# Performance work log

Hardware: AMD Instinct MI355X
Metric: run time of the kernel (lower is better)

## Reference

```python
import jax, jax.numpy as jnp
import numpy as np

B, SEQ, DIM, HEADS = 2, 2048, 512, 8
HD = DIM // HEADS
RANK, DFF = 128, 1024
TAU_MEM, TAU_ADAPT, SLOPE, EPS = 0.99, 0.95, 25.0, 1e-6
THRESH, ADAPT_STRENGTH = 0.5, 0.1
TREE_LEVELS = int(np.log2(SEQ))  # 11


def rmsnorm(x, w, eps=EPS):
    return x * jax.lax.rsqrt(jnp.mean(x * x, axis=-1, keepdims=True) + eps) * w


def rope_cos_sin(seq, hd):
    inv = 1.0 / (10000.0 ** (jnp.arange(0, hd, 2, dtype=jnp.float32) / hd))
    f = jnp.arange(seq, dtype=jnp.float32)[:, None] * inv[None, :]  # [S, hd/2]
    emb = jnp.concatenate([f, f], axis=-1)  # [S, hd]
    return jnp.cos(emb), jnp.sin(emb)


def apply_rope(x, cos, sin):
    # x: [B, H, S, hd]; rotate-half formulation
    x1, x2 = jnp.split(x, 2, axis=-1)
    return x * cos + jnp.concatenate([-x2, x1], axis=-1) * sin


def setup_inputs() -> dict:
    key = jax.random.key(0)
    ks = jax.random.split(key, 12)
    w = lambda k, shape, fan: (jax.random.normal(k, shape, jnp.float32) / np.sqrt(fan))
    return {
        "x": jax.random.normal(ks[0], (B, SEQ, DIM), jnp.float32),
        "norm_w": jnp.ones((DIM,), jnp.float32),
        "wq": w(ks[1], (DIM, DIM), DIM),
        "wk": w(ks[2], (DIM, DIM), DIM),
        "wv": w(ks[3], (DIM, DIM), DIM),
        "wo": w(ks[4], (DIM, DIM), DIM),
        "lat_w": w(ks[5], (SEQ, SEQ), SEQ),
        "bt": jnp.full((DIM,), THRESH, jnp.float32),
        "as_w": jnp.full((DIM,), ADAPT_STRENGTH, jnp.float32),
        "gate_w": w(ks[6], (DIM, DIM), DIM),
        "tnorm1_w": jnp.ones((DIM,), jnp.float32),
        "tnorm2_w": jnp.ones((DIM,), jnp.float32),
        "ffn_norm_w": jnp.ones((DIM,), jnp.float32),
        "u_w": w(ks[7], (DIM, RANK), DIM),
        "v_w": w(ks[8], (RANK, 2 * DFF), RANK),
        "down_w": w(ks[9], (DFF, DIM), DFF),
    }


def reference(x, norm_w, wq, wk, wv, wo, lat_w, bt, as_w, gate_w,
              tnorm1_w, tnorm2_w, ffn_norm_w, u_w, v_w, down_w):
    Bx, S, D = x.shape
    # --- pre-norm + QKV projections (base_proj) ---
    h = rmsnorm(x, norm_w)
    q = (h @ wq.T).reshape(Bx, S, HEADS, HD).transpose(0, 2, 1, 3)  # [B,H,S,hd]
    k = (h @ wk.T).reshape(Bx, S, HEADS, HD).transpose(0, 2, 1, 3)
    v = (h @ wv.T).reshape(Bx, S, HEADS, HD).transpose(0, 2, 1, 3)
    # --- RoPE ---
    cos, sin = rope_cos_sin(S, HD)
    q = apply_rope(q, cos, sin)
    k = apply_rope(k, cos, sin)
    # --- causal self-attention ---
    scores = jnp.einsum("bhqd,bhkd->bhqk", q, k) / np.sqrt(HD)
    causal = jnp.tril(jnp.ones((S, S), bool))
    scores = jnp.where(causal, scores, jnp.float32(-1e9))
    attn = jnp.einsum("bhqk,bhkd->bhqd", jax.nn.softmax(scores, axis=-1), v)
    attn = attn.transpose(0, 2, 1, 3).reshape(Bx, S, D) @ wo.T
    # --- causal lateral mixing across sequence ---
    mixed = jnp.einsum("ts,bsd->btd", jnp.tril(lat_w), attn)
    # --- ALIF spiking recurrence over the sequence (soft surrogate spike) ---
    def alif_step(carry, i_t):
        vmem, ad = carry
        vmem = TAU_MEM * vmem + i_t
        th = bt + as_w * ad
        spike = jax.nn.sigmoid(SLOPE * (vmem - th))
        vmem = vmem - spike * th          # soft reset
        ad = TAU_ADAPT * ad + spike        # threshold adaptation
        return (vmem, ad), spike
    init = (jnp.zeros((Bx, D), x.dtype), jnp.zeros((Bx, D), x.dtype))
    _, spikes = jax.lax.scan(alif_step, init, mixed.transpose(1, 0, 2))
    spikes = spikes.transpose(1, 0, 2)  # [B,S,D]
    # --- fused addadd residual ---
    h2 = x + mixed + spikes
    # --- binary-tree cell recursion to a root summary ---
    s = h2
    for _ in range(TREE_LEVELS):
        raw = s[:, 0::2, :] + s[:, 1::2, :]         # pairwise sums (raw_sums)
        res = 0.5 * raw                              # residual / prev_s surrogate
        n = rmsnorm(raw, tnorm1_w)
        g = jax.nn.sigmoid(n @ gate_w.T)
        s = rmsnorm(g * n + (1.0 - g) * res, tnorm2_w)
    h3 = h2 + s[:, 0:1, :]  # broadcast root back over the sequence
    # --- low-rank SwiGLU FFN ---
    hn = rmsnorm(h3, ffn_norm_w)
    up = (hn @ u_w) @ v_w                 # [B,S,2*DFF]
    a, b = jnp.split(up, 2, axis=-1)
    ffn = (jax.nn.silu(a) * b) @ down_w   # [B,S,D]
    return h3 + ffn
```

## Files before the change

### kernel.cpp

```cpp
#include <hip/hip_runtime.h>
#include <math.h>

#define BB 2
#define SS 2048
#define DD 512
#define HH 8
#define HDD 64
#define RANKK 128
#define DFFF 1024

typedef short bf16x8 __attribute__((ext_vector_type(8)));
typedef float f32x4 __attribute__((ext_vector_type(4)));

__device__ __forceinline__ short f2b(float f) {
  union { float f; unsigned u; } v; v.f = f;
  unsigned r = v.u + 0x7FFF + ((v.u >> 16) & 1);
  return (short)(r >> 16);
}
__device__ __forceinline__ float b2f(short s) {
  union { unsigned u; float f; } v; v.u = ((unsigned)(unsigned short)s) << 16;
  return v.f;
}

__device__ __forceinline__ void gll16(const void* g, void* l) {
  __builtin_amdgcn_global_load_lds(
      (const __attribute__((address_space(1))) unsigned int*)g,
      (__attribute__((address_space(3))) unsigned int*)l, 16, 0, 0);
}

__device__ __forceinline__ float wsum(float v) {
#pragma unroll
  for (int off = 32; off > 0; off >>= 1) v += __shfl_xor(v, off, 64);
  return v;
}

__global__ void splitw(const float* __restrict__ in, short* __restrict__ hi,
                       short* __restrict__ lo, int n) {
  int i = (blockIdx.x * 256 + threadIdx.x) * 4;
  if (i >= n) return;
  float4 v = *(const float4*)(in + i);
  short4 h4, l4;
  h4.x = f2b(v.x); l4.x = f2b(v.x - b2f(h4.x));
  h4.y = f2b(v.y); l4.y = f2b(v.y - b2f(h4.y));
  h4.z = f2b(v.z); l4.z = f2b(v.z - b2f(h4.z));
  h4.w = f2b(v.w); l4.w = f2b(v.w - b2f(h4.w));
  *(short4*)(hi + i) = h4;
  *(short4*)(lo + i) = l4;
}

__global__ void cvtb(const float* __restrict__ in, short* __restrict__ out, int n) {
  int i = (blockIdx.x * 256 + threadIdx.x) * 4;
  if (i >= n) return;
  float4 v = *(const float4*)(in + i);
  short4 o; o.x = f2b(v.x); o.y = f2b(v.y); o.z = f2b(v.z); o.w = f2b(v.w);
  *(short4*)(out + i) = o;
}

__global__ void sum2(const float* __restrict__ a, const float* __restrict__ bq,
                     float* __restrict__ o) {
  int i = (blockIdx.x * 256 + threadIdx.x) * 4;
  float4 va = *(const float4*)(a + i);
  float4 vb = *(const float4*)(bq + i);
  float4 vo = {va.x + vb.x, va.y + vb.y, va.z + vb.z, va.w + vb.w};
  *(float4*)(o + i) = vo;
}

__global__ void transp_cvt(const float* __restrict__ in, short* __restrict__ out,
                           int R, int C) {
  __shared__ float t[32][33];
  int c0 = blockIdx.x * 32, r0 = blockIdx.y * 32;
#pragma unroll
  for (int i = 0; i < 4; i++) {
    int idx = threadIdx.x + i * 256;
    int r = idx >> 5, c = idx & 31;
    t[r][c] = in[(size_t)(r0 + r) * C + c0 + c];
  }
  __syncthreads();
#pragma unroll
  for (int i = 0; i < 4; i++) {
    int idx = threadIdx.x + i * 256;
    int cc = idx >> 5, rr = idx & 31;
    out[(size_t)(c0 + cc) * R + r0 + rr] = f2b(t[rr][cc]);
  }
}

__global__ void rmsnorm_hl(const float* __restrict__ x, const float* __restrict__ w,
                           short* __restrict__ oh, short* __restrict__ ol, int rows) {
  int wid = blockIdx.x * 4 + (threadIdx.x >> 6);
  int lane = threadIdx.x & 63;
  if (wid >= rows) return;
  const float* xp = x + (size_t)wid * DD + lane * 8;
  float4 a = *(const float4*)xp;
  float4 b = *(const float4*)(xp + 4);
  float ss = a.x*a.x + a.y*a.y + a.z*a.z + a.w*a.w
           + b.x*b.x + b.y*b.y + b.z*b.z + b.w*b.w;
  ss = wsum(ss);
  float r = rsqrtf(ss * (1.0f / DD) + 1e-6f);
  const float* wp = w + lane * 8;
  float4 wa = *(const float4*)wp, wb = *(const float4*)(wp + 4);
  float o8[8] = {a.x*r*wa.x, a.y*r*wa.y, a.z*r*wa.z, a.w*r*wa.w,
                 b.x*r*wb.x, b.y*r*wb.y, b.z*r*wb.z, b.w*r*wb.w};
  short hv[8], lv[8];
#pragma unroll
  for (int i = 0; i < 8; i++) { hv[i] = f2b(o8[i]); lv[i] = f2b(o8[i] - b2f(hv[i])); }
  short* op = oh + (size_t)wid * DD + lane * 8;
  short* lp = ol + (size_t)wid * DD + lane * 8;
  *(short4*)op = make_short4(hv[0], hv[1], hv[2], hv[3]);
  *(short4*)(op + 4) = make_short4(hv[4], hv[5], hv[6], hv[7]);
  *(short4*)lp = make_short4(lv[0], lv[1], lv[2], lv[3]);
  *(short4*)(lp + 4) = make_short4(lv[4], lv[5], lv[6], lv[7]);
}

template <bool SPL, int OM, bool ROPE>
__global__ __launch_bounds__(256) void ggemm(const short* __restrict__ Ah_g,
                                             const short* __restrict__ Al_g,
                                             const short* __restrict__ Bh_g,
                                             const short* __restrict__ Bl_g,
                                             const float* __restrict__ ADD,
                                             void* __restrict__ C, void* __restrict__ C2,
                                             int M, int N, int K) {
  __shared__ short Ahs[128 * 32];
  __shared__ short Bhs[128 * 32];
  __shared__ short Als[SPL ? 128 * 32 : 8];
  __shared__ short Bls[SPL ? 128 * 32 : 8];
  const int tid = threadIdx.x, l = tid & 63, w = tid >> 6;
  const int wr = (w >> 1) * 64, wc = (w & 1) * 64;
  const int bm = blockIdx.y * 128, bn = blockIdx.x * 128;
  f32x4 acc[4][4] = {};
  for (int k0 = 0; k0 < K; k0 += 32) {
#pragma unroll
    for (int p = 0; p < 2; p++) {
      int row = p * 64 + (tid >> 2), g = tid & 3;
      int swz = (g ^ ((row >> 1) & 3)) * 8;
      gll16(Ah_g + (size_t)(bm + row) * K + k0 + swz, Ahs + p * 2048 + tid * 8);
      gll16(Bh_g + (size_t)(bn + row) * K + k0 + swz, Bhs + p * 2048 + tid * 8);
      if (SPL) {
        gll16(Al_g + (size_t)(bm + row) * K + k0 + swz, Als + p * 2048 + tid * 8);
        gll16(Bl_g + (size_t)(bn + row) * K + k0 + swz, Bls + p * 2048 + tid * 8);
      }
    }
    __syncthreads();
    bf16x8 ah[4], bh[4], al[4], bl[4];
#pragma unroll
    for (int m = 0; m < 4; m++) {
      int r = wr + m * 16 + (l & 15);
      int go = (((l >> 4) ^ ((r >> 1) & 3)) << 3);
      ah[m] = *(const bf16x8*)(Ahs + r * 32 + go);
      if (SPL) al[m] = *(const bf16x8*)(Als + r * 32 + go);
    }
#pragma unroll
    for (int n = 0; n < 4; n++) {
      int r = wc + n * 16 + (l & 15);
      int go = (((l >> 4) ^ ((r >> 1) & 3)) << 3);
      bh[n] = *(const bf16x8*)(Bhs + r * 32 + go);
      if (SPL) bl[n] = *(const bf16x8*)(Bls + r * 32 + go);
    }
#pragma unroll
    for (int m = 0; m < 4; m++)
#pragma unroll
      for (int n = 0; n < 4; n++) {
        acc[m][n] = __builtin_amdgcn_mfma_f32_16x16x32_bf16(ah[m], bh[n], acc[m][n], 0, 0, 0);
        if (SPL) {
          acc[m][n] = __builtin_amdgcn_mfma_f32_16x16x32_bf16(ah[m], bl[n], acc[m][n], 0, 0, 0);
          acc[m][n] = __builtin_amdgcn_mfma_f32_16x16x32_bf16(al[m], bh[n], acc[m][n], 0, 0, 0);
        }
      }
    __syncthreads();
  }
  const int ll = l & 15, lg4 = (l >> 4) * 4;
  if (ROPE) {
#pragma unroll
    for (int m = 0; m < 4; m++)
#pragma unroll
      for (int n = 0; n < 2; n++) {
        int i_ = n * 16 + ll;
        float inv = exp2f(-(float)i_ * (13.287712379549449f / 32.0f));
#pragma unroll
        for (int j = 0; j < 4; j++) {
          int gm = bm + wr + m * 16 + lg4 + j;
          int s = gm & (SS - 1);
          float ang = (float)s * inv;
          float sn, cs;
          sincosf(ang, &sn, &cs);
          float v1 = acc[m][n][j], v2 = acc[m][n + 2][j];
          acc[m][n][j]     = v1 * cs - v2 * sn;
          acc[m][n + 2][j] = v2 * cs + v1 * sn;
        }
      }
  }
#pragma unroll
  for (int m = 0; m < 4; m++)
#pragma unroll
    for (int n = 0; n < 4; n++) {
      int gn = bn + wc + n * 16 + ll;
#pragma unroll
      for (int j = 0; j < 4; j++) {
        int gm = bm + wr + m * 16 + lg4 + j;
        if (gm >= M || gn >= N) continue;
        float v = acc[m][n][j];
        if (OM == 0) {
          ((float*)C)[(size_t)gm * N + gn] = v;
        } else if (OM == 1) {
          ((short*)C)[(size_t)gm * N + gn] = f2b(v);
        } else if (OM == 6) {
          size_t off = (size_t)gm * N + gn;
          ((float*)C)[off] = v + ADD[off];
        } else {
          short hi = f2b(v);
          short lo = f2b(v - b2f(hi));
          int b = gm >> 11, s = gm & (SS - 1);
          int hh2 = gn >> 6, d = gn & 63;
          size_t off;
          if (OM == 2)      off = (((size_t)(b * HH + hh2)) * SS + s) * 64 + d;
          else if (OM == 3) off = (((size_t)(b * HH + hh2)) * 64 + d) * SS + s;
          else              off = ((size_t)(b * DD) + gn) * SS + s;
          ((short*)C)[off] = hi;
          ((short*)C2)[off] = lo;
        }
      }
    }
}

__global__ __launch_bounds__(256) void qkv_g(const short* __restrict__ Ah_g,
                                             const short* __restrict__ Al_g,
                                             const short* __restrict__ wh0, const short* __restrict__ wl0,
                                             const short* __restrict__ wh1, const short* __restrict__ wl1,
                                             const short* __restrict__ wh2, const short* __restrict__ wl2,
                                             short* __restrict__ c0h, short* __restrict__ c0l,
                                             short* __restrict__ c1h, short* __restrict__ c1l,
                                             short* __restrict__ c2h, short* __restrict__ c2l) {
  const int z = blockIdx.z;
  const short* Bh_g = (z == 0) ? wh0 : (z == 1) ? wh1 : wh2;
  const short* Bl_g = (z == 0) ? wl0 : (z == 1) ? wl1 : wl2;
  short* Ch = (z == 0) ? c0h : (z == 1) ? c1h : c2h;
  short* Cl = (z == 0) ? c0l : (z == 1) ? c1l : c2l;
  const int K = DD;
  __shared__ short Ahs[128 * 32];
  __shared__ short Bhs[128 * 32];
  __shared__ short Als[128 * 32];
  __shared__ short Bls[128 * 32];
  const int tid = threadIdx.x, l = tid & 63, w = tid >> 6;
  const int wr = (w >> 1) * 64, wc = (w & 1) * 64;
  const int bm = blockIdx.y * 128, bn = blockIdx.x * 128;
  f32x4 acc[4][4] = {};
  for (int k0 = 0; k0 < K; k0 += 32) {
#pragma unroll
    for (int p = 0; p < 2; p++) {
      int row = p * 64 + (tid >> 2), g = tid & 3;
      int swz = (g ^ ((row >> 1) & 3)) * 8;
      gll16(Ah_g + (size_t)(bm + row) * K + k0 + swz, Ahs + p * 2048 + tid * 8);
      gll16(Bh_g + (size_t)(bn + row) * K + k0 + swz, Bhs + p * 2048 + tid * 8);
      gll16(Al_g + (size_t)(bm + row) * K + k0 + swz, Als + p * 2048 + tid * 8);
      gll16(Bl_g + (size_t)(bn + row) * K + k0 + swz, Bls + p * 2048 + tid * 8);
    }
    __syncthreads();
    bf16x8 ah[4], bh[4], al[4], bl[4];
#pragma unroll
    for (int m = 0; m < 4; m++) {
      int r = wr + m * 16 + (l & 15);
      int go = (((l >> 4) ^ ((r >> 1) & 3)) << 3);
      ah[m] = *(const bf16x8*)(Ahs + r * 32 + go);
      al[m] = *(const bf16x8*)(Als + r * 32 + go);
    }
#pragma unroll
    for (int n = 0; n < 4; n++) {
      int r = wc + n * 16 + (l & 15);
      int go = (((l >> 4) ^ ((r >> 1) & 3)) << 3);
      bh[n] = *(const bf16x8*)(Bhs + r * 32 + go);
      bl[n] = *(const bf16x8*)(Bls + r * 32 + go);
    }
#pragma unroll
    for (int m = 0; m < 4; m++)
#pragma unroll
      for (int n = 0; n < 4; n++) {
        acc[m][n] = __builtin_amdgcn_mfma_f32_16x16x32_bf16(ah[m], bh[n], acc[m][n], 0, 0, 0);
        acc[m][n] = __builtin_amdgcn_mfma_f32_16x16x32_bf16(ah[m], bl[n], acc[m][n], 0, 0, 0);
        acc[m][n] = __builtin_amdgcn_mfma_f32_16x16x32_bf16(al[m], bh[n], acc[m][n], 0, 0, 0);
      }
    __syncthreads();
  }
  const int ll = l & 15, lg4 = (l >> 4) * 4;
  if (z < 2) {
#pragma unroll
    for (int m = 0; m < 4; m++)
#pragma unroll
      for (int n = 0; n < 2; n++) {
        int i_ = n * 16 + ll;
        float inv = exp2f(-(float)i_ * (13.287712379549449f / 32.0f));
#pragma unroll
        for (int j = 0; j < 4; j++) {
          int gm = bm + wr + m * 16 + lg4 + j;
          int s = gm & (SS - 1);
          float ang = (float)s * inv;
          float sn, cs;
          sincosf(ang, &sn, &cs);
          float v1 = acc[m][n][j], v2 = acc[m][n + 2][j];
          acc[m][n][j]     = v1 * cs - v2 * sn;
          acc[m][n + 2][j] = v2 * cs + v1 * sn;
        }
      }
  }
#pragma unroll
  for (int m = 0; m < 4; m++)
#pragma unroll
    for (int n = 0; n < 4; n++) {
      int gn = bn + wc + n * 16 + ll;
#pragma unroll
      for (int j = 0; j < 4; j++) {
        int gm = bm + wr + m * 16 + lg4 + j;
        float v = acc[m][n][j];
        short hi = f2b(v);
        short lo = f2b(v - b2f(hi));
        int b = gm >> 11, s = gm & (SS - 1);
        int hh2 = gn >> 6, d = gn & 63;
        size_t off = (z < 2) ? ((((size_t)(b * HH + hh2)) * SS + s) * 64 + d)
                             : ((((size_t)(b * HH + hh2)) * 64 + d) * SS + s);
        Ch[off] = hi;
        Cl[off] = lo;
      }
    }
}

__global__ __launch_bounds__(256) void lat_g(const float* __restrict__ lat,
                                             const short* __restrict__ bTh,
                                             const short* __restrict__ bTl,
                                             float* __restrict__ P0,
                                             float* __restrict__ P1) {
  const int zb = blockIdx.z >> 1;
  const int half = blockIdx.z & 1;
  bTh += (size_t)zb * DD * SS;
  bTl += (size_t)zb * DD * SS;
  float* Cc = (half == 0 ? P0 : P1) + (size_t)zb * DD * SS;
  __shared__ short Ah[128 * 32];
  __shared__ short Al[128 * 32];
  __shared__ short Bh[128 * 32];
  __shared__ short Bl[128 * 32];
  const int tid = threadIdx.x, l = tid & 63, w = tid >> 6;
  const int wr = (w >> 1) * 64, wc = (w & 1) * 64;
  const int bm = blockIdx.y * 128, bn = blockIdx.x * 128;
  const int T = blockIdx.y + 1;
  const int h0 = (T + 1) >> 1;
  const int kbeg = (half == 0) ? 0 : h0 * 128;
  const int kend = (half == 0) ? h0 * 128 : T * 128;
  f32x4 acc[4][4] = {};
  const int ll = l & 15, lg4 = (l >> 4) * 4;
  for (int k0 = kbeg; k0 < kend; k0 += 32) {
#pragma unroll
    for (int p = 0; p < 2; p++) {
      int row = p * 64 + (tid >> 2), g = tid & 3;
      int swz = (g ^ ((row >> 1) & 3)) * 8;
      gll16(bTh + (size_t)(bn + row) * SS + k0 + swz, Bh + p * 2048 + tid * 8);
      gll16(bTl + (size_t)(bn + row) * SS + k0 + swz, Bl + p * 2048 + tid * 8);
    }
#pragma unroll
    for (int i = 0; i < 4; i++) {
      int lin = i * 256 + tid;
      int row = lin >> 3, f4 = lin & 7;
      int gr = bm + row;
      float4 v = *(const float4*)(lat + (size_t)gr * SS + k0 + f4 * 4);
      int kc = k0 + f4 * 4;
      if (kc + 0 > gr) v.x = 0.0f;
      if (kc + 1 > gr) v.y = 0.0f;
      if (kc + 2 > gr) v.z = 0.0f;
      if (kc + 3 > gr) v.w = 0.0f;
      int off = row * 32 + (((f4 >> 1) ^ ((row >> 1) & 3)) << 3) + (f4 & 1) * 4;
      short4 hh, lo;
      hh.x = f2b(v.x); lo.x = f2b(v.x - b2f(hh.x));
      hh.y = f2b(v.y); lo.y = f2b(v.y - b2f(hh.y));
      hh.z = f2b(v.z); lo.z = f2b(v.z - b2f(hh.z));
      hh.w = f2b(v.w); lo.w = f2b(v.w - b2f(hh.w));
      *(short4*)(Ah + off) = hh;
      *(short4*)(Al + off) = lo;
    }
    __syncthreads();
    bf16x8 ah[4], bh[4], al[4], bl[4];
#pragma unroll
    for (int m = 0; m < 4; m++) {
      int r = wr + m * 16 + (l & 15);
      int go = (((l >> 4) ^ ((r >> 1) & 3)) << 3);
      ah[m] = *(const bf16x8*)(Ah + r * 32 + go);
      al[m] = *(const bf16x8*)(Al + r * 32 + go);
    }
#pragma unroll
    for (int n = 0; n < 4; n++) {
      int r = wc + n * 16 + (l & 15);
      int go = (((l >> 4) ^ ((r >> 1) & 3)) << 3);
      bh[n] = *(const bf16x8*)(Bh + r * 32 + go);
      bl[n] = *(const bf16x8*)(Bl + r * 32 + go);
    }
#pragma unroll
    for (int m = 0; m < 4; m++)
#pragma unroll
      for (int n = 0; n < 4; n++) {
        acc[m][n] = __builtin_amdgcn_mfma_f32_16x16x32_bf16(ah[m], bh[n], acc[m][n], 0, 0, 0);
        acc[m][n] = __builtin_amdgcn_mfma_f32_16x16x32_bf16(ah[m], bl[n], acc[m][n], 0, 0, 0);
        acc[m][n] = __builtin_amdgcn_mfma_f32_16x16x32_bf16(al[m], bh[n], acc[m][n], 0, 0, 0);
      }
    __syncthreads();
  }
#pragma unroll
  for (int m = 0; m < 4; m++)
#pragma unroll
    for (int n = 0; n < 4; n++) {
      int gn = bn + wc + n * 16 + ll;
#pragma unroll
      for (int j = 0; j < 4; j++) {
        int gm = bm + wr + m * 16 + lg4 + j;
        size_t off = ((size_t)((gm >> 5) * 512 + gn)) * 32 + ((gm + gn) & 31);
        Cc[off] = acc[m][n][j];
      }
    }
}

__global__ __launch_bounds__(256) void attn_g(const short* __restrict__ qh,
                                              const short* __restrict__ ql,
                                              const short* __restrict__ kh,
                                              const short* __restrict__ kl,
                                              const short* __restrict__ vh,
                                              const short* __restrict__ vl,
                                              short* __restrict__ aho,
                                              short* __restrict__ alo) {
  const int h = blockIdx.y, b = blockIdx.z;
  const int qt = (b == 0) ? (int)blockIdx.x : 31 - (int)blockIdx.x;
  const int q0 = qt * 64;
  const int tid = threadIdx.x, w = tid >> 6, l = tid & 63;
  const int lg = l >> 4, ll = l & 15;
  __shared__ short Kh[64 * 64], Kl[64 * 64];
  __shared__ short Vh[64 * 64], Vl[64 * 64];
  __shared__ short Ph[64 * 64], Pl[64 * 64];
  const size_t bh = (size_t)(b * HH + h);

  const int qr = q0 + w * 16 + ll;
  const short* qbh = qh + (bh * SS + qr) * 64;
  const short* qbl = ql + (bh * SS + qr) * 64;
  bf16x8 qfh[2], qfl[2];
#pragma unroll
  for (int ks = 0; ks < 2; ks++) {
    qfh[ks] = *(const bf16x8*)(qbh + (ks * 4 + lg) * 8);
    qfl[ks] = *(const bf16x8*)(qbl + (ks * 4 + lg) * 8);
  }

  f32x4 o[4] = {};
  float mrow[4] = {-1e30f, -1e30f, -1e30f, -1e30f};
  float lsum[4] = {};
  const int qrow0 = q0 + w * 16 + lg * 4;
  const int ntiles = qt + 1;

  for (int kt = 0; kt < ntiles; kt++) {
#pragma unroll
    for (int p = 0; p < 2; p++) {
      int row = p * 32 + (tid >> 3), g = tid & 7;
      int sw = ((g ^ (row & 7)) << 3);
      size_t krow = (bh * SS + kt * 64 + row) * 64;
      size_t vrow = (bh * 64 + row) * SS + kt * 64;
      gll16(kh + krow + sw, Kh + p * 2048 + tid * 8);
      gll16(kl + krow + sw, Kl + p * 2048 + tid * 8);
      gll16(vh + vrow + sw, Vh + p * 2048 + tid * 8);
      gll16(vl + vrow + sw, Vl + p * 2048 + tid * 8);
    }
    __syncthreads();

    f32x4 sv[4] = {};
#pragma unroll
    for (int nf = 0; nf < 4; nf++) {
      int r = nf * 16 + ll;
#pragma unroll
      for (int ks = 0; ks < 2; ks++) {
        int g = (ks * 4 + lg) ^ (r & 7);
        bf16x8 khf = *(const bf16x8*)(Kh + r * 64 + g * 8);
        bf16x8 klf = *(const bf16x8*)(Kl + r * 64 + g * 8);
        sv[nf] = __builtin_amdgcn_mfma_f32_16x16x32_bf16(qfh[ks], khf, sv[nf], 0, 0, 0);
        sv[nf] = __builtin_amdgcn_mfma_f32_16x16x32_bf16(qfh[ks], klf, sv[nf], 0, 0, 0);
        sv[nf] = __builtin_amdgcn_mfma_f32_16x16x32_bf16(qfl[ks], khf, sv[nf], 0, 0, 0);
      }
    }
#pragma unroll
    for (int nf = 0; nf < 4; nf++) {
      int kpos = kt * 64 + nf * 16 + ll;
#pragma unroll
      for (int j = 0; j < 4; j++) {
        float v = sv[nf][j] * 0.125f;
        sv[nf][j] = (kpos > qrow0 + j) ? -1e30f : v;
      }
    }
    float cf[4];
#pragma unroll
    for (int j = 0; j < 4; j++) {
      float r = fmaxf(fmaxf(sv[0][j], sv[1][j]), fmaxf(sv[2][j], sv[3][j]));
      r = fmaxf(r, __shfl_xor(r, 1)); r = fmaxf(r, __shfl_xor(r, 2));
      r = fmaxf(r, __shfl_xor(r, 4)); r = fmaxf(r, __shfl_xor(r, 8));
      float mn = fmaxf(mrow[j], r);
      cf[j] = __expf(mrow[j] - mn);
      mrow[j] = mn;
    }
    float ps[4] = {};
#pragma unroll
    for (int nf = 0; nf < 4; nf++)
#pragma unroll
      for (int j = 0; j < 4; j++) {
        float p = __expf(sv[nf][j] - mrow[j]);
        sv[nf][j] = p;
        ps[j] += p;
      }
#pragma unroll
    for (int j = 0; j < 4; j++) {
      float r = ps[j];
      r += __shfl_xor(r, 1); r += __shfl_xor(r, 2);
      r += __shfl_xor(r, 4); r += __shfl_xor(r, 8);
      lsum[j] = lsum[j] * cf[j] + r;
    }
#pragma unroll
    for (int nf = 0; nf < 4; nf++)
#pragma unroll
      for (int j = 0; j < 4; j++) o[nf][j] *= cf[j];
#pragma unroll
    for (int nf = 0; nf < 4; nf++)
#pragma unroll
      for (int j = 0; j < 4; j++) {
        int rowP = w * 16 + lg * 4 + j;
        int col = nf * 16 + ll;
        int off = rowP * 64 + (((col >> 3) ^ (rowP & 7)) << 3) + (col & 7);
        float p = sv[nf][j];
        short hi = f2b(p);
        Ph[off] = hi;
        Pl[off] = f2b(p - b2f(hi));
      }
    __syncthreads();
    bf16x8 pfh[2], pfl[2];
    {
      int rowA = w * 16 + ll;
#pragma unroll
      for (int ks = 0; ks < 2; ks++) {
        int g = (ks * 4 + lg) ^ (rowA & 7);
        pfh[ks] = *(const bf16x8*)(Ph + rowA * 64 + g * 8);
        pfl[ks] = *(const bf16x8*)(Pl + rowA * 64 + g * 8);
      }
    }
#pragma unroll
    for (int nf = 0; nf < 4; nf++) {
      int r = nf * 16 + ll;
#pragma unroll
      for (int ks = 0; ks < 2; ks++) {
        int g = (ks * 4 + lg) ^ (r & 7);
        bf16x8 vhf = *(const bf16x8*)(Vh + r * 64 + g * 8);
        bf16x8 vlf = *(const bf16x8*)(Vl + r * 64 + g * 8);
        o[nf] = __builtin_amdgcn_mfma_f32_16x16x32_bf16(pfh[ks], vhf, o[nf], 0, 0, 0);
        o[nf] = __builtin_amdgcn_mfma_f32_16x16x32_bf16(pfh[ks], vlf, o[nf], 0, 0, 0);
        o[nf] = __builtin_amdgcn_mfma_f32_16x16x32_bf16(pfl[ks], vhf, o[nf], 0, 0, 0);
      }
    }
    __syncthreads();
  }
  float inv[4];
#pragma unroll
  for (int j = 0; j < 4; j++) inv[j] = 1.0f / lsum[j];
#pragma unroll
  for (int nf = 0; nf < 4; nf++)
#pragma unroll
    for (int j = 0; j < 4; j++) {
      float v = o[nf][j] * inv[j];
      short hi = f2b(v);
      size_t off = ((size_t)(b * SS + qrow0 + j)) * DD + h * HDD + nf * 16 + ll;
      aho[off] = hi;
      alo[off] = f2b(v - b2f(hi));
    }
}

#define ACH 32
__global__ __launch_bounds__(64) void tsa_alif6(const float* __restrict__ mixedS,
                                                const float* __restrict__ bt,
                                                const float* __restrict__ asw,
                                                float* __restrict__ spikesS) {
  __shared__ float lds[2][ACH * 64];
  const int t = threadIdx.x;
  const int tid = blockIdx.x * 64 + t;
  const int b = tid >> 9, d = tid & 511;
  const int d0 = d & ~63;
  const float btd = bt[d], asd = asw[d];
  const float C = 36.06737602222409f;
  const float bt36 = btd * C, as36 = asd * C;
  const float bt99 = 0.99f * btd, as99 = 0.99f * asd;
  const size_t bbase = (size_t)b * DD * SS;
  {
    const float* g0 = mixedS + bbase + (size_t)d0 * 32;
#pragma unroll
    for (int i = 0; i < 8; i++) gll16(g0 + i * 256 + t * 4, &lds[0][i * 256 + t * 4]);
  }
  float vR = 0.0f, ad = 0.0f;
  for (int c = 0; c < SS / ACH; c++) {
    const int cur = c & 1;
    __syncthreads();
    if (c + 1 < SS / ACH) {
      const float* gq = mixedS + bbase + ((size_t)((c + 1) * 512 + d0)) * 32;
#pragma unroll
      for (int i = 0; i < 8; i++) gll16(gq + i * 256 + t * 4, &lds[cur ^ 1][i * 256 + t * 4]);
    }
    float m[ACH];
#pragma unroll
    for (int j = 0; j < ACH; j++) m[j] = lds[cur][t * 32 + ((j + t) & 31)];
    vR += m[0];
    float sO[ACH];
#pragma unroll
    for (int j = 0; j < ACH; j++) {
      float thC = fmaf(ad, as36, bt36);
      float th99 = fmaf(ad, as99, bt99);
      float arg = fmaf(vR, -C, thC);
      float e = exp2f(arg);
      float s = __builtin_amdgcn_rcpf(1.0f + e);
      sO[j] = s;
      float pre = (j + 1 < ACH) ? fmaf(0.99f, vR, m[j + 1]) : (0.99f * vR);
      vR = fmaf(-th99, s, pre);
      ad = fmaf(0.95f, ad, s);
    }
#pragma unroll
    for (int j = 0; j < ACH; j++) lds[cur][t * 32 + ((j + t) & 31)] = sO[j];
    __syncthreads();
    float* so = spikesS + bbase + ((size_t)(c * 512 + d0)) * 32;
#pragma unroll
    for (int i = 0; i < 8; i++) {
      float4 v4 = *(const float4*)&lds[cur][i * 256 + t * 4];
      *(float4*)(so + i * 256 + t * 4) = v4;
    }
  }
}

__global__ __launch_bounds__(256) void fuse_h2(const float* __restrict__ x,
                                               const float* __restrict__ mixedS,
                                               const float* __restrict__ spikesS,
                                               float* __restrict__ h2) {
  const int s0 = blockIdx.x * 64, d0 = blockIdx.y * 64, b = blockIdx.z;
  __shared__ float t[64][65];
  const int dl = threadIdx.x >> 2;
  const int grp = threadIdx.x & 3;
  const size_t bbase = (size_t)b * DD * SS;
#pragma unroll
  for (int i = 0; i < 16; i++) {
    int sl = grp * 16 + i;
    int sg = s0 + sl;
    size_t off = bbase + ((size_t)((sg >> 5) * 512 + d0 + dl)) * 32 + ((sg + dl) & 31);
    t[dl][sl] = mixedS[off] + spikesS[off];
  }
  __syncthreads();
#pragma unroll
  for (int k = 0; k < 4; k++) {
    int sl = threadIdx.x >> 2;
    int dl2 = (threadIdx.x & 3) * 16 + k * 4;
    size_t off = ((size_t)(b * SS + s0 + sl)) * DD + d0 + dl2;
    float4 xv = *(const float4*)(x + off);
    float4 o;
    o.x = xv.x + t[dl2 + 0][sl];
    o.y = xv.y + t[dl2 + 1][sl];
    o.z = xv.z + t[dl2 + 2][sl];
    o.w = xv.w + t[dl2 + 3][sl];
    *(float4*)(h2 + off) = o;
  }
}

__global__ void tree_reduce_b(const float* __restrict__ sin_, const float* __restrict__ tn1,
                              short* __restrict__ nb, int Sn) {
  int wid = blockIdx.x * 4 + (threadIdx.x >> 6);
  int lane = threadIdx.x & 63;
  int rows = BB * Sn;
  if (wid >= rows) return;
  int b = wid / Sn, j = wid - b * Sn;
  const float* r0 = sin_ + ((size_t)(b * 2 * Sn + 2 * j)) * DD + lane * 8;
  const float* r1 = r0 + DD;
  float4 a0 = *(const float4*)r0, a1 = *(const float4*)(r0 + 4);
  float4 b0 = *(const float4*)r1, b1 = *(const float4*)(r1 + 4);
  float ra[8] = {a0.x + b0.x, a0.y + b0.y, a0.z + b0.z, a0.w + b0.w,
                 a1.x + b1.x, a1.y + b1.y, a1.z + b1.z, a1.w + b1.w};
  float ss = 0.0f;
#pragma unroll
  for (int i = 0; i < 8; i++) ss += ra[i] * ra[i];
  ss = wsum(ss);
  float rms = rsqrtf(ss * (1.0f / DD) + 1e-6f);
  const float* wp = tn1 + lane * 8;
  float4 wa = *(const float4*)wp, wb = *(const float4*)(wp + 4);
  float wv8[8] = {wa.x, wa.y, wa.z, wa.w, wb.x, wb.y, wb.z, wb.w};
  short* np = nb + (size_t)wid * DD + lane * 8;
  short4 n0, n1;
  n0.x = f2b(ra[0]*rms*wv8[0]); n0.y = f2b(ra[1]*rms*wv8[1]);
  n0.z = f2b(ra[2]*rms*wv8[2]); n0.w = f2b(ra[3]*rms*wv8[3]);
  n1.x = f2b(ra[4]*rms*wv8[4]); n1.y = f2b(ra[5]*rms*wv8[5]);
  n1.z = f2b(ra[6]*rms*wv8[6]); n1.w = f2b(ra[7]*rms*wv8[7]);
  *(short4*)np = n0;
  *(short4*)(np + 4) = n1;
}

__global__ void tree_combine_b(const float* __restrict__ g, const short* __restrict__ nb,
                               const float* __restrict__ sin_, const float* __restrict__ tn2,
                               float* __restrict__ sout, int Sn) {
  int wid = blockIdx.x * 4 + (threadIdx.x >> 6);
  int lane = threadIdx.x & 63;
  int rows = BB * Sn;
  if (wid >= rows) return;
  int b = wid / Sn, j = wid - b * Sn;
  const float* r0 = sin_ + ((size_t)(b * 2 * Sn + 2 * j)) * DD + lane * 8;
  const float* r1 = r0 + DD;
  float4 a0 = *(const float4*)r0, a1 = *(const float4*)(r0 + 4);
  float4 b0 = *(const float4*)r1, b1 = *(const float4*)(r1 + 4);
  float res[8] = {0.5f*(a0.x + b0.x), 0.5f*(a0.y + b0.y), 0.5f*(a0.z + b0.z), 0.5f*(a0.w + b0.w),
                  0.5f*(a1.x + b1.x), 0.5f*(a1.y + b1.y), 0.5f*(a1.z + b1.z), 0.5f*(a1.w + b1.w)};
  size_t base = (size_t)wid * DD + lane * 8;
  float t[8];
  float ss = 0.0f;
#pragma unroll
  for (int i = 0; i < 8; i++) {
    float gg = 1.0f / (1.0f + expf(-g[base + i]));
    float tv = gg * b2f(nb[base + i]) + (1.0f - gg) * res[i];
    t[i] = tv;
    ss += tv * tv;
  }
  ss = wsum(ss);
  float rms = rsqrtf(ss * (1.0f / DD) + 1e-6f);
#pragma unroll
  for (int i = 0; i < 8; i++) sout[base + i] = t[i] * rms * tn2[lane * 8 + i];
}

__global__ void h3hn_b(const float* __restrict__ h2, const float* __restrict__ root,
                       const float* __restrict__ fw, float* __restrict__ h3,
                       short* __restrict__ hn) {
  int wid = blockIdx.x * 4 + (threadIdx.x >> 6);
  int lane = threadIdx.x & 63;
  int b = wid >> 11;
  size_t base = (size_t)wid * DD + lane * 8;
  const float* rp = root + (size_t)b * DD + lane * 8;
  float t[8];
  float ss = 0.0f;
#pragma unroll
  for (int i = 0; i < 8; i++) {
    float tv = h2[base + i] + rp[i];
    t[i] = tv;
    ss += tv * tv;
    h3[base + i] = tv;
  }
  ss = wsum(ss);
  float rms = rsqrtf(ss * (1.0f / DD) + 1e-6f);
#pragma unroll
  for (int i = 0; i < 8; i++) hn[base + i] = f2b(t[i] * rms * fw[lane * 8 + i]);
}

__global__ __launch_bounds__(256) void upgate_g(const short* __restrict__ A,
                                                const short* __restrict__ Bv,
                                                short* __restrict__ ffa) {
  __shared__ short Ahs[128 * 32];
  __shared__ short B1s[128 * 32];
  __shared__ short B2s[128 * 32];
  const int tid = threadIdx.x, l = tid & 63, w = tid >> 6;
  const int wr = (w >> 1) * 64, wc = (w & 1) * 64;
  const int bm = blockIdx.y * 128, bn = blockIdx.x * 128;
  f32x4 acc1[4][4] = {}, acc2[4][4] = {};
  for (int k0 = 0; k0 < RANKK; k0 += 32) {
#pragma unroll
    for (int p = 0; p < 2; p++) {
      int row = p * 64 + (tid >> 2), g = tid & 3;
      int swz = (g ^ ((row >> 1) & 3)) * 8;
      gll16(A + (size_t)(bm + row) * RANKK + k0 + swz, Ahs + p * 2048 + tid * 8);
      gll16(Bv + (size_t)(bn + row) * RANKK + k0 + swz, B1s + p * 2048 + tid * 8);
      gll16(Bv + (size_t)(DFFF + bn + row) * RANKK + k0 + swz, B2s + p * 2048 + tid * 8);
    }
    __syncthreads();
    bf16x8 ah[4], b1[4], b2[4];
#pragma unroll
    for (int m = 0; m < 4; m++) {
      int r = wr + m * 16 + (l & 15);
      int go = (((l >> 4) ^ ((r >> 1) & 3)) << 3);
      ah[m] = *(const bf16x8*)(Ahs + r * 32 + go);
    }
#pragma unroll
    for (int n = 0; n < 4; n++) {
      int r = wc + n * 16 + (l & 15);
      int go = (((l >> 4) ^ ((r >> 1) & 3)) << 3);
      b1[n] = *(const bf16x8*)(B1s + r * 32 + go);
      b2[n] = *(const bf16x8*)(B2s + r * 32 + go);
    }
#pragma unroll
    for (int m = 0; m < 4; m++)
#pragma unroll
      for (int n = 0; n < 4; n++) {
        acc1[m][n] = __builtin_amdgcn_mfma_f32_16x16x32_bf16(ah[m], b1[n], acc1[m][n], 0, 0, 0);
        acc2[m][n] = __builtin_amdgcn_mfma_f32_16x16x32_bf16(ah[m], b2[n], acc2[m][n], 0, 0, 0);
      }
    __syncthreads();
  }
#pragma unroll
  for (int m = 0; m < 4; m++)
#pragma unroll
    for (int n = 0; n < 4; n++) {
      int gn = bn + wc + n * 16 + (l & 15);
#pragma unroll
      for (int j = 0; j < 4; j++) {
        int gm = bm + wr + m * 16 + (l >> 4) * 4 + j;
        float a = acc1[m][n][j];
        float s = a / (1.0f + __expf(-a));
        ffa[(size_t)gm * DFFF + gn] = f2b(s * acc2[m][n][j]);
      }
    }
}

extern "C" void kernel_launch(void* const* d_in, const int* in_sizes, int n_in,
                              void* d_out, int out_size, void* d_ws, size_t ws_size,
                              hipStream_t stream) {
  const float* x   = (const float*)d_in[0];
  const float* nw  = (const float*)d_in[1];
  const float* wq  = (const float*)d_in[2];
  const float* wk  = (const float*)d_in[3];
  const float* wv  = (const float*)d_in[4];
  const float* wo  = (const float*)d_in[5];
  const float* lat = (const float*)d_in[6];
  const float* btp = (const float*)d_in[7];
  const float* asw = (const float*)d_in[8];
  const float* gw  = (const float*)d_in[9];
  const float* tn1 = (const float*)d_in[10];
  const float* tn2 = (const float*)d_in[11];
  const float* fnw = (const float*)d_in[12];
  const float* uw  = (const float*)d_in[13];
  const float* vw  = (const float*)d_in[14];
  const float* dw  = (const float*)d_in[15];
  float* out = (float*)d_out;
  char* W = (char*)d_ws;
  const size_t MB = 1u << 20;

  short* h_hi = (short*)(W);
  short* h_lo = (short*)(W + 4 * MB);
  short* attn_hi = h_hi;
  short* attn_lo = h_lo;
  short* nb = (short*)(W);
  float* gb = (float*)(W + 2 * MB);
  short* q_hi = (short*)(W + 8 * MB);
  short* q_lo = (short*)(W + 12 * MB);
  short* apT_hi = q_hi;
  short* apT_lo = q_lo;
  float* spikesS = (float*)(W + 8 * MB);
  float* s0 = (float*)(W + 8 * MB);
  float* s1 = (float*)(W + 12 * MB);
  short* k_hi = (short*)(W + 16 * MB);
  short* k_lo = (short*)(W + 20 * MB);
  float* latP1 = (float*)(W + 16 * MB);
  short* hn = (short*)(W + 16 * MB);
  short* t1 = (short*)(W + 20 * MB);
  short* v_hi = (short*)(W + 24 * MB);
  short* v_lo = (short*)(W + 28 * MB);
  float* h2 = (float*)(W + 24 * MB);
  short* ffa = (short*)(W + 24 * MB);
  float* latP0 = (float*)(W + 32 * MB);
  short* gwb = (short*)(W + 32 * MB);
  short* uwT = gwb + 262144;
  short* vwT = uwT + 65536;
  short* dwT = vwT + 262144;

  short* wqh = (short*)out;
  short* wql = wqh + 262144;
  short* wkh = wql + 262144;
  short* wkl = wkh + 262144;
  short* wvh = wkl + 262144;
  short* wvl = wvh + 262144;
  short* woh = wvl + 262144;
  short* wol = woh + 262144;

  const int rows = BB * SS;

  splitw<<<256, 256, 0, stream>>>(wq, wqh, wql, DD * DD);
  splitw<<<256, 256, 0, stream>>>(wk, wkh, wkl, DD * DD);
  splitw<<<256, 256, 0, stream>>>(wv, wvh, wvl, DD * DD);
  splitw<<<256, 256, 0, stream>>>(wo, woh, wol, DD * DD);

  rmsnorm_hl<<<rows / 4, 256, 0, stream>>>(x, nw, h_hi, h_lo, rows);

  qkv_g<<<dim3(4, 32, 3), 256, 0, stream>>>(h_hi, h_lo,
                                            wqh, wql, wkh, wkl, wvh, wvl,
                                            q_hi, q_lo, k_hi, k_lo, v_hi, v_lo);

  attn_g<<<dim3(32, HH, BB), 256, 0, stream>>>(q_hi, q_lo, k_hi, k_lo, v_hi, v_lo,
                                               attn_hi, attn_lo);

  ggemm<true, 4, false><<<dim3(4, 32), 256, 0, stream>>>(
      attn_hi, attn_lo, woh, wol, nullptr, apT_hi, apT_lo, rows, DD, DD);

  lat_g<<<dim3(4, 16, 4), 256, 0, stream>>>(lat, apT_hi, apT_lo, latP0, latP1);

  sum2<<<(BB * DD * SS / 4) / 256, 256, 0, stream>>>(latP0, latP1, latP0);

  tsa_alif6<<<16, 64, 0, stream>>>(latP0, btp, asw, spikesS);
  fuse_h2<<<dim3(32, 8, 2), 256, 0, stream>>>(x, latP0, spikesS, h2);

  cvtb<<<256, 256, 0, stream>>>(gw, gwb, DD * DD);
  transp_cvt<<<dim3(4, 16), 256, 0, stream>>>(uw, uwT, DD, RANKK);
  transp_cvt<<<dim3(64, 4), 256, 0, stream>>>(vw, vwT, RANKK, 2 * DFFF);
  transp_cvt<<<dim3(16, 32), 256, 0, stream>>>(dw, dwT, DFFF, DD);

  const float* sin_ = h2;
  for (int lvl = 0; lvl < 11; lvl++) {
    int Sn = 1024 >> lvl;
    int r2 = BB * Sn;
    float* sout = (lvl & 1) ? s1 : s0;
    tree_reduce_b<<<(r2 + 3) / 4, 256, 0, stream>>>(sin_, tn1, nb, Sn);
    ggemm<false, 0, false><<<dim3(4, (r2 + 127) / 128), 256, 0, stream>>>(
        nb, nullptr, gwb, nullptr, nullptr, gb, nullptr, r2, DD, DD);
    tree_combine_b<<<(r2 + 3) / 4, 256, 0, stream>>>(gb, nb, sin_, tn2, sout, Sn);
    sin_ = sout;
  }

  h3hn_b<<<rows / 4, 256, 0, stream>>>(h2, sin_, fnw, out, hn);

  ggemm<false, 1, false><<<dim3(1, 32), 256, 0, stream>>>(
      hn, nullptr, uwT, nullptr, nullptr, t1, nullptr, rows, RANKK, DD);
  upgate_g<<<dim3(8, 32), 256, 0, stream>>>(t1, vwT, ffa);
  ggemm<false, 6, false><<<dim3(4, 32), 256, 0, stream>>>(
      ffa, nullptr, dwT, nullptr, out, out, nullptr, rows, DD, DFFF);
}
```

Baseline: 686.1 us.

## Pre-split lat weights, drop P-lo term in attention, fuse partial-sum into ALIF

Combines several changes. The four weight-split launches become one grid-z kernel. The masked lat matrix is split to bf16 hi/lo once up front, so lat_g loads both halves asynchronously instead of converting in-loop. The sum2 kernel is removed and the two K-halves are instead added inside the ALIF scan and fuse_h2. Attention drops the low-order bf16 term of P and one MFMA per step, which trades accuracy for less compute and less LDS use.

After: 712.7 us. 3.9% more time.

```diff
diff --git a/kernel.cpp b/kernel.cpp
--- a/kernel.cpp
+++ b/kernel.cpp
@@ -34,10 +34,16 @@
   return v;
 }
 
-__global__ void splitw(const float* __restrict__ in, short* __restrict__ hi,
-                       short* __restrict__ lo, int n) {
+__global__ void splitw4(const float* __restrict__ w0, const float* __restrict__ w1,
+                        const float* __restrict__ w2, const float* __restrict__ w3,
+                        short* h0, short* l0_, short* h1, short* l1_,
+                        short* h2_, short* l2_, short* h3_, short* l3_) {
+  const int z = blockIdx.z;
+  const float* in = (z == 0) ? w0 : (z == 1) ? w1 : (z == 2) ? w2 : w3;
+  short* hi = (z == 0) ? h0 : (z == 1) ? h1 : (z == 2) ? h2_ : h3_;
+  short* lo = (z == 0) ? l0_ : (z == 1) ? l1_ : (z == 2) ? l2_ : l3_;
   int i = (blockIdx.x * 256 + threadIdx.x) * 4;
-  if (i >= n) return;
+  if (i >= DD * DD) return;
   float4 v = *(const float4*)(in + i);
   short4 h4, l4;
   h4.x = f2b(v.x); l4.x = f2b(v.x - b2f(h4.x));
@@ -48,21 +54,31 @@
   *(short4*)(lo + i) = l4;
 }
 
+__global__ void splitlat(const float* __restrict__ lat, short* __restrict__ hi,
+                         short* __restrict__ lo) {
+  int i = (blockIdx.x * 256 + threadIdx.x) * 4;
+  int r = i >> 11;
+  int c = i & 2047;
+  float4 v = *(const float4*)(lat + i);
+  if (c + 0 > r) v.x = 0.0f;
+  if (c + 1 > r) v.y = 0.0f;
+  if (c + 2 > r) v.z = 0.0f;
+  if (c + 3 > r) v.w = 0.0f;
+  short4 h4, l4;
+  h4.x = f2b(v.x); l4.x = f2b(v.x - b2f(h4.x));
+  h4.y = f2b(v.y); l4.y = f2b(v.y - b2f(h4.y));
+  h4.z = f2b(v.z); l4.z = f2b(v.z - b2f(h4.z));
+  h4.w = f2b(v.w); l4.w = f2b(v.w - b2f(h4.w));
+  *(short4*)(hi + i) = h4;
+  *(short4*)(lo + i) = l4;
+}
+
 __global__ void cvtb(const float* __restrict__ in, short* __restrict__ out, int n) {
   int i = (blockIdx.x * 256 + threadIdx.x) * 4;
   if (i >= n) return;
   float4 v = *(const float4*)(in + i);
   short4 o; o.x = f2b(v.x); o.y = f2b(v.y); o.z = f2b(v.z); o.w = f2b(v.w);
   *(short4*)(out + i) = o;
-}
-
-__global__ void sum2(const float* __restrict__ a, const float* __restrict__ bq,
-                     float* __restrict__ o) {
-  int i = (blockIdx.x * 256 + threadIdx.x) * 4;
-  float4 va = *(const float4*)(a + i);
-  float4 vb = *(const float4*)(bq + i);
-  float4 vo = {va.x + vb.x, va.y + vb.y, va.z + vb.z, va.w + vb.w};
-  *(float4*)(o + i) = vo;
 }
 
 __global__ void transp_cvt(const float* __restrict__ in, short* __restrict__ out,
@@ -321,7 +337,8 @@
     }
 }
 
-__global__ __launch_bounds__(256) void lat_g(const float* __restrict__ lat,
+__global__ __launch_bounds__(256) void lat_g(const short* __restrict__ lath,
+                                             const short* __restrict__ latl,
                                              const short* __restrict__ bTh,
                                              const short* __restrict__ bTl,
                                              float* __restrict__ P0,
@@ -351,26 +368,8 @@
       int swz = (g ^ ((row >> 1) & 3)) * 8;
       gll16(bTh + (size_t)(bn + row) * SS + k0 + swz, Bh + p * 2048 + tid * 8);
       gll16(bTl + (size_t)(bn + row) * SS + k0 + swz, Bl + p * 2048 + tid * 8);
-    }
-#pragma unroll
-    for (int i = 0; i < 4; i++) {
-      int lin = i * 256 + tid;
-      int row = lin >> 3, f4 = lin & 7;
-      int gr = bm + row;
-      float4 v = *(const float4*)(lat + (size_t)gr * SS + k0 + f4 * 4);
-      int kc = k0 + f4 * 4;
-      if (kc + 0 > gr) v.x = 0.0f;
-      if (kc + 1 > gr) v.y = 0.0f;
-      if (kc + 2 > gr) v.z = 0.0f;
-      if (kc + 3 > gr) v.w = 0.0f;
-      int off = row * 32 + (((f4 >> 1) ^ ((row >> 1) & 3)) << 3) + (f4 & 1) * 4;
-      short4 hh, lo;
-      hh.x = f2b(v.x); lo.x = f2b(v.x - b2f(hh.x));
-      hh.y = f2b(v.y); lo.y = f2b(v.y - b2f(hh.y));
-      hh.z = f2b(v.z); lo.z = f2b(v.z - b2f(hh.z));
-      hh.w = f2b(v.w); lo.w = f2b(v.w - b2f(hh.w));
-      *(short4*)(Ah + off) = hh;
-      *(short4*)(Al + off) = lo;
+      gll16(lath + (size_t)(bm + row) * SS + k0 + swz, Ah + p * 2048 + tid * 8);
+      gll16(latl + (size_t)(bm + row) * SS + k0 + swz, Al + p * 2048 + tid * 8);
     }
     __syncthreads();
     bf16x8 ah[4], bh[4], al[4], bl[4];
@@ -427,7 +426,7 @@
   const int lg = l >> 4, ll = l & 15;
   __shared__ short Kh[64 * 64], Kl[64 * 64];
   __shared__ short Vh[64 * 64], Vl[64 * 64];
-  __shared__ short Ph[64 * 64], Pl[64 * 64];
+  __shared__ short Ph[64 * 64];
   const size_t bh = (size_t)(b * HH + h);
 
   const int qr = q0 + w * 16 + ll;
@@ -520,20 +519,16 @@
         int rowP = w * 16 + lg * 4 + j;
         int col = nf * 16 + ll;
         int off = rowP * 64 + (((col >> 3) ^ (rowP & 7)) << 3) + (col & 7);
-        float p = sv[nf][j];
-        short hi = f2b(p);
-        Ph[off] = hi;
-        Pl[off] = f2b(p - b2f(hi));
-      }
-    __syncthreads();
-    bf16x8 pfh[2], pfl[2];
+        Ph[off] = f2b(sv[nf][j]);
+      }
+    __syncthreads();
+    bf16x8 pfh[2];
     {
       int rowA = w * 16 + ll;
 #pragma unroll
       for (int ks = 0; ks < 2; ks++) {
         int g = (ks * 4 + lg) ^ (rowA & 7);
         pfh[ks] = *(const bf16x8*)(Ph + rowA * 64 + g * 8);
-        pfl[ks] = *(const bf16x8*)(Pl + rowA * 64 + g * 8);
       }
     }
 #pragma unroll
@@ -546,7 +541,6 @@
         bf16x8 vlf = *(const bf16x8*)(Vl + r * 64 + g * 8);
         o[nf] = __builtin_amdgcn_mfma_f32_16x16x32_bf16(pfh[ks], vhf, o[nf], 0, 0, 0);
         o[nf] = __builtin_amdgcn_mfma_f32_16x16x32_bf16(pfh[ks], vlf, o[nf], 0, 0, 0);
-        o[nf] = __builtin_amdgcn_mfma_f32_16x16x32_bf16(pfl[ks], vhf, o[nf], 0, 0, 0);
       }
     }
     __syncthreads();
@@ -567,11 +561,13 @@
 }
 
 #define ACH 32
-__global__ __launch_bounds__(64) void tsa_alif6(const float* __restrict__ mixedS,
+__global__ __launch_bounds__(64) void tsa_alif7(const float* __restrict__ P0,
+                                                const float* __restrict__ P1,
                                                 const float* __restrict__ bt,
                                                 const float* __restrict__ asw,
                                                 float* __restrict__ spikesS) {
-  __shared__ float lds[2][ACH * 64];
+  __shared__ float ldsA[2][ACH * 64];
+  __shared__ float ldsB[2][ACH * 64];
   const int t = threadIdx.x;
   const int tid = blockIdx.x * 64 + t;
   const int b = tid >> 9, d = tid & 511;
@@ -581,23 +577,37 @@
   const float bt36 = btd * C, as36 = asd * C;
   const float bt99 = 0.99f * btd, as99 = 0.99f * asd;
   const size_t bbase = (size_t)b * DD * SS;
+  const float* pa = P0 + bbase;
+  const float* pb = P1 + bbase;
+  float* sp = spikesS + bbase;
   {
-    const float* g0 = mixedS + bbase + (size_t)d0 * 32;
-#pragma unroll
-    for (int i = 0; i < 8; i++) gll16(g0 + i * 256 + t * 4, &lds[0][i * 256 + t * 4]);
+    const float* gA = pa + (size_t)d0 * 32;
+    const float* gB = pb + (size_t)d0 * 32;
+#pragma unroll
+    for (int i = 0; i < 8; i++) {
+      gll16(gA + i * 256 + t * 4, &ldsA[0][i * 256 + t * 4]);
+      gll16(gB + i * 256 + t * 4, &ldsB[0][i * 256 + t * 4]);
+    }
   }
   float vR = 0.0f, ad = 0.0f;
   for (int c = 0; c < SS / ACH; c++) {
     const int cur = c & 1;
     __syncthreads();
     if (c + 1 < SS / ACH) {
-      const float* gq = mixedS + bbase + ((size_t)((c + 1) * 512 + d0)) * 32;
-#pragma unroll
-      for (int i = 0; i < 8; i++) gll16(gq + i * 256 + t * 4, &lds[cur ^ 1][i * 256 + t * 4]);
+      const float* gA = pa + ((size_t)((c + 1) * 512 + d0)) * 32;
+      const float* gB = pb + ((size_t)((c + 1) * 512 + d0)) * 32;
+#pragma unroll
+      for (int i = 0; i < 8; i++) {
+        gll16(gA + i * 256 + t * 4, &ldsA[cur ^ 1][i * 256 + t * 4]);
+        gll16(gB + i * 256 + t * 4, &ldsB[cur ^ 1][i * 256 + t * 4]);
+      }
     }
     float m[ACH];
 #pragma unroll
-    for (int j = 0; j < ACH; j++) m[j] = lds[cur][t * 32 + ((j + t) & 31)];
+    for (int j = 0; j < ACH; j++) {
+      int idx = t * 32 + ((j + t) & 31);
+      m[j] = ldsA[cur][idx] + ldsB[cur][idx];
+    }
     vR += m[0];
     float sO[ACH];
 #pragma unroll
@@ -613,19 +623,20 @@
       ad = fmaf(0.95f, ad, s);
     }
 #pragma unroll
-    for (int j = 0; j < ACH; j++) lds[cur][t * 32 + ((j + t) & 31)] = sO[j];
-    __syncthreads();
-    float* so = spikesS + bbase + ((size_t)(c * 512 + d0)) * 32;
+    for (int j = 0; j < ACH; j++) ldsA[cur][t * 32 + ((j + t) & 31)] = sO[j];
+    __syncthreads();
+    float* so = sp + ((size_t)(c * 512 + d0)) * 32;
 #pragma unroll
     for (int i = 0; i < 8; i++) {
-      float4 v4 = *(const float4*)&lds[cur][i * 256 + t * 4];
+      float4 v4 = *(const float4*)&ldsA[cur][i * 256 + t * 4];
       *(float4*)(so + i * 256 + t * 4) = v4;
     }
   }
 }
 
 __global__ __launch_bounds__(256) void fuse_h2(const float* __restrict__ x,
-                                               const float* __restrict__ mixedS,
+                                               const float* __restrict__ P0,
+                                               const float* __restrict__ P1,
                                                const float* __restrict__ spikesS,
                                                float* __restrict__ h2) {
   const int s0 = blockIdx.x * 64, d0 = blockIdx.y * 64, b = blockIdx.z;
@@ -638,7 +649,7 @@
     int sl = grp * 16 + i;
     int sg = s0 + sl;
     size_t off = bbase + ((size_t)((sg >> 5) * 512 + d0 + dl)) * 32 + ((sg + dl) & 31);
-    t[dl][sl] = mixedS[off] + spikesS[off];
+    t[dl][sl] = P0[off] + P1[off] + spikesS[off];
   }
   __syncthreads();
 #pragma unroll
@@ -825,6 +836,7 @@
   short* h_lo = (short*)(W + 4 * MB);
   short* attn_hi = h_hi;
   short* attn_lo = h_lo;
+  float* latP0 = (float*)(W);
   short* nb = (short*)(W);
   float* gb = (float*)(W + 2 * MB);
   short* q_hi = (short*)(W + 8 * MB);
@@ -836,14 +848,15 @@
   float* s1 = (float*)(W + 12 * MB);
   short* k_hi = (short*)(W + 16 * MB);
   short* k_lo = (short*)(W + 20 * MB);
-  float* latP1 = (float*)(W + 16 * MB);
+  short* lath = (short*)(W + 16 * MB);
   short* hn = (short*)(W + 16 * MB);
   short* t1 = (short*)(W + 20 * MB);
   short* v_hi = (short*)(W + 24 * MB);
   short* v_lo = (short*)(W + 28 * MB);
+  short* latl = (short*)(W + 24 * MB);
   float* h2 = (float*)(W + 24 * MB);
   short* ffa = (short*)(W + 24 * MB);
-  float* latP0 = (float*)(W + 32 * MB);
+  float* latP1 = (float*)(W + 32 * MB);
   short* gwb = (short*)(W + 32 * MB);
   short* uwT = gwb + 262144;
   short* vwT = uwT + 65536;
@@ -860,10 +873,8 @@
 
   const int rows = BB * SS;
 
-  splitw<<<256, 256, 0, stream>>>(wq, wqh, wql, DD * DD);
-  splitw<<<256, 256, 0, stream>>>(wk, wkh, wkl, DD * DD);
-  splitw<<<256, 256, 0, stream>>>(wv, wvh, wvl, DD * DD);
-  splitw<<<256, 256, 0, stream>>>(wo, woh, wol, DD * DD);
+  splitw4<<<dim3(256, 1, 4), 256, 0, stream>>>(wq, wk, wv, wo,
+                                               wqh, wql, wkh, wkl, wvh, wvl, woh, wol);
 
   rmsnorm_hl<<<rows / 4, 256, 0, stream>>>(x, nw, h_hi, h_lo, rows);
 
@@ -877,12 +888,12 @@
   ggemm<true, 4, false><<<dim3(4, 32), 256, 0, stream>>>(
       attn_hi, attn_lo, woh, wol, nullptr, apT_hi, apT_lo, rows, DD, DD);
 
-  lat_g<<<dim3(4, 16, 4), 256, 0, stream>>>(lat, apT_hi, apT_lo, latP0, latP1);
-
-  sum2<<<(BB * DD * SS / 4) / 256, 256, 0, stream>>>(latP0, latP1, latP0);
-
-  tsa_alif6<<<16, 64, 0, stream>>>(latP0, btp, asw, spikesS);
-  fuse_h2<<<dim3(32, 8, 2), 256, 0, stream>>>(x, latP0, spikesS, h2);
+  splitlat<<<4096, 256, 0, stream>>>(lat, lath, latl);
+
+  lat_g<<<dim3(4, 16, 4), 256, 0, stream>>>(lath, latl, apT_hi, apT_lo, latP0, latP1);
+
+  tsa_alif7<<<16, 64, 0, stream>>>(latP0, latP1, btp, asw, spikesS);
+  fuse_h2<<<dim3(32, 8, 2), 256, 0, stream>>>(x, latP0, latP1, spikesS, h2);
 
   cvtb<<<256, 256, 0, stream>>>(gw, gwb, DD * DD);
   transp_cvt<<<dim3(4, 16), 256, 0, stream>>>(uw, uwT, DD, RANKK);
```
